# Optimization experiments

Hardware: AMD Instinct MI355X
Metric: run time of the kernel (lower is better)

Reference implementation:

```python
import jax, jax.numpy as jnp
import numpy as np

LN_EPS = 1e-5   # torch nn.LayerNorm default
OPM_EPS = 1e-3  # module eps


def _layer_norm(x, gamma, beta):
    mu = jnp.mean(x, axis=-1, keepdims=True)
    var = jnp.var(x, axis=-1, keepdims=True)
    return (x - mu) * jax.lax.rsqrt(var + LN_EPS) * gamma + beta


def setup_inputs() -> dict:
    key = jax.random.key(0)
    ks = jax.random.split(key, 4)
    S, N, c_m, c_h, c_z = 128, 384, 256, 32, 128
    return {
        "m": jax.random.normal(ks[0], (S, N, c_m), dtype=jnp.float32),
        "mask": jnp.ones((S, N), dtype=jnp.float32),
        "ln_gamma": jnp.ones((c_m,), dtype=jnp.float32),
        "ln_beta": jnp.zeros((c_m,), dtype=jnp.float32),
        "w1": jax.random.normal(ks[1], (c_m, c_h), dtype=jnp.float32) / np.sqrt(c_m),
        "b1": jnp.zeros((c_h,), dtype=jnp.float32),
        "w2": jax.random.normal(ks[2], (c_m, c_h), dtype=jnp.float32) / np.sqrt(c_m),
        "b2": jnp.zeros((c_h,), dtype=jnp.float32),
        "w_out": jax.random.normal(ks[3], (c_h * c_h, c_z), dtype=jnp.float32) / np.sqrt(c_h * c_h),
        "b_out": jnp.zeros((c_z,), dtype=jnp.float32),
    }


def reference(m, mask, ln_gamma, ln_beta, w1, b1, w2, b2, w_out, b_out):
    # m: [S, N, C_m], mask: [S, N]
    ln = _layer_norm(m, ln_gamma, ln_beta)                      # [S, N, C_m]
    a = (ln @ w1 + b1) * mask[..., None]                        # [S, N, C_h]
    b = (ln @ w2 + b2) * mask[..., None]                        # [S, N, C_h]
    a = jnp.swapaxes(a, -2, -3)                                 # [N, S, C_h]
    b = jnp.swapaxes(b, -2, -3)                                 # [N, S, C_h]
    norm = jnp.einsum('si,sj->ij', mask, mask)[..., None] + OPM_EPS  # [N, N, 1]
    outer = jnp.einsum('isc,jsd->ijcd', a, b)                   # [N, N, C_h, C_h]
    outer = outer.reshape(outer.shape[:-2] + (-1,))             # [N, N, C_h^2]
    out = outer @ w_out + b_out                                 # [N, N, C_z]
    return out / norm
```

## Files before the change

kernel.cpp:

```cpp
#include <hip/hip_runtime.h>
#include <hip/hip_bf16.h>

#define S_ 128
#define N_ 384
#define CM 256
#define CH 32
#define CZ 128

typedef __attribute__((ext_vector_type(8))) __bf16 bf16x8;
typedef __attribute__((ext_vector_type(4))) float f32x4;

union pack4 { __hip_bfloat16 h[4]; uint2 u; };

__global__ __launch_bounds__(384) void k_prep(const float* __restrict__ w1,
                                              const float* __restrict__ w2,
                                              const float* __restrict__ wout,
                                              const float* __restrict__ mask,
                                              __hip_bfloat16* __restrict__ wt12,
                                              __hip_bfloat16* __restrict__ woutT,
                                              float* __restrict__ RN)
{
    const int b = blockIdx.x, t = threadIdx.x;
    if (b < 64) {
        if (t < 256) {
            const float* w = (b < CH) ? w1 : w2;
            wt12[b * CM + t] = __float2bfloat16(w[(size_t)t * CH + (b & 31)]);
        }
    } else if (b < 192) {
        const int z = b - 64;
        for (int cd = t; cd < CH*CH; cd += 384)
            woutT[(size_t)z * (CH*CH) + cd] = __float2bfloat16(wout[(size_t)cd * CZ + z]);
    } else {
        const int i = b - 192, j = t;
        float acc = 0.f;
        #pragma unroll 8
        for (int s = 0; s < S_; ++s)
            acc += mask[s*N_ + i] * mask[s*N_ + j];
        RN[i*N_ + j] = 1.0f / (acc + 1e-3f);
    }
}

#define LNR 264
__global__ __launch_bounds__(256) void k_lnp(
    const float* __restrict__ m, const float* __restrict__ mask,
    const float* __restrict__ gamma, const float* __restrict__ beta,
    const float* __restrict__ b1, const float* __restrict__ b2,
    const __hip_bfloat16* __restrict__ wt12,
    __hip_bfloat16* __restrict__ At, __hip_bfloat16* __restrict__ Bt)
{
    __shared__ __hip_bfloat16 lnS[128 * LNR];
    __shared__ float msk[128];
    const int n0 = blockIdx.x * 16, s0 = blockIdx.y * 8;
    const int t = threadIdx.x, wave = t >> 6, lane = t & 63;
    const int l15 = lane & 15, quad = lane >> 4;

    if (t < 128) msk[t] = mask[(s0 + (t & 7))*N_ + n0 + (t >> 3)];

    float4 ga[4], be4[4];
    #pragma unroll
    for (int u = 0; u < 4; ++u) {
        ga[u]  = ((const float4*)gamma)[u*16 + l15];
        be4[u] = ((const float4*)beta )[u*16 + l15];
    }

    for (int it = 0; it < 8; ++it) {
        const int row = wave*32 + it*4 + quad;
        const int n = row >> 3, s = row & 7;
        const float4* src = (const float4*)(m + ((size_t)((s0+s)*N_ + n0 + n)) * CM);
        float4 x[4];
        #pragma unroll
        for (int u = 0; u < 4; ++u) x[u] = src[u*16 + l15];

        float sum = 0.f, ssq = 0.f;
        #pragma unroll
        for (int u = 0; u < 4; ++u) {
            sum += x[u].x + x[u].y + x[u].z + x[u].w;
            ssq += x[u].x*x[u].x + x[u].y*x[u].y + x[u].z*x[u].z + x[u].w*x[u].w;
        }
        #pragma unroll
        for (int off = 8; off >= 1; off >>= 1) {
            sum += __shfl_xor(sum, off, 64);
            ssq += __shfl_xor(ssq, off, 64);
        }
        const float mean = sum * (1.0f/CM);
        const float var  = ssq * (1.0f/CM) - mean*mean;
        const float rstd = rsqrtf(var + 1e-5f);

        #pragma unroll
        for (int u = 0; u < 4; ++u) {
            pack4 pk;
            pk.h[0] = __float2bfloat16((x[u].x - mean)*rstd*ga[u].x + be4[u].x);
            pk.h[1] = __float2bfloat16((x[u].y - mean)*rstd*ga[u].y + be4[u].y);
            pk.h[2] = __float2bfloat16((x[u].z - mean)*rstd*ga[u].z + be4[u].z);
            pk.h[3] = __float2bfloat16((x[u].w - mean)*rstd*ga[u].w + be4[u].w);
            *(uint2*)&lnS[row*LNR + (u*16 + l15)*4] = pk.u;
        }
    }
    __syncthreads();

    f32x4 acc[2][4];
    const f32x4 z4 = {0.f,0.f,0.f,0.f};
    #pragma unroll
    for (int mt = 0; mt < 2; ++mt)
        #pragma unroll
        for (int nt = 0; nt < 4; ++nt) acc[mt][nt] = z4;

    #pragma unroll
    for (int kk = 0; kk < 8; ++kk) {
        bf16x8 a0 = *(const bf16x8*)&lnS[(wave*32      + l15)*LNR + kk*32 + quad*8];
        bf16x8 a1 = *(const bf16x8*)&lnS[(wave*32 + 16 + l15)*LNR + kk*32 + quad*8];
        #pragma unroll
        for (int nt = 0; nt < 4; ++nt) {
            bf16x8 wv = *(const bf16x8*)&wt12[(size_t)(nt*16 + l15)*CM + kk*32 + quad*8];
            acc[0][nt] = __builtin_amdgcn_mfma_f32_16x16x32_bf16(a0, wv, acc[0][nt], 0,0,0);
            acc[1][nt] = __builtin_amdgcn_mfma_f32_16x16x32_bf16(a1, wv, acc[1][nt], 0,0,0);
        }
    }

    #pragma unroll
    for (int nt = 0; nt < 4; ++nt) {
        const int ncol = nt*16 + l15;
        const int sel = ncol >> 5, c = ncol & 31;
        const float bias = sel ? b2[c] : b1[c];
        __hip_bfloat16* dst = sel ? Bt : At;
        #pragma unroll
        for (int mt = 0; mt < 2; ++mt) {
            const int rowb = wave*32 + mt*16 + quad*4;
            const int n_loc = rowb >> 3, s_loc = rowb & 7;
            pack4 pk;
            #pragma unroll
            for (int r = 0; r < 4; ++r)
                pk.h[r] = __float2bfloat16((acc[mt][nt][r] + bias) * msk[rowb + r]);
            *(uint2*)&dst[((size_t)(n0 + n_loc)*CH + c)*S_ + s0 + s_loc] = pk.u;
        }
    }
}

#define OR 1160
__global__ __launch_bounds__(512) void k_opm(
    const __hip_bfloat16* __restrict__ At, const __hip_bfloat16* __restrict__ Bt,
    const float* __restrict__ RN, const __hip_bfloat16* __restrict__ woutT,
    const float* __restrict__ bout, float* __restrict__ out)
{
    __shared__ __hip_bfloat16 O[64 * OR];
    const int t = threadIdx.x;
    const int wave = t >> 6, lane = t & 63;
    const int l15 = lane & 15, quad = lane >> 4;
    const int i0 = blockIdx.x * 8, j0 = blockIdx.y * 8;
    const int mhalf = wave & 1, nquad = wave >> 1;

    f32x4 acc[4][8];
    const f32x4 z4 = {0.f,0.f,0.f,0.f};
    #pragma unroll
    for (int nt = 0; nt < 4; ++nt)
        #pragma unroll
        for (int mt = 0; mt < 8; ++mt) acc[nt][mt] = z4;

    const __hip_bfloat16* Ag[8];
    #pragma unroll
    for (int mt = 0; mt < 8; ++mt) {
        const int Mrow = mhalf*128 + mt*16 + l15;
        Ag[mt] = At + ((size_t)(i0 + (Mrow >> 5)) * CH + (Mrow & 31)) * S_ + quad*8;
    }
    const __hip_bfloat16* Bg[4];
    #pragma unroll
    for (int nt = 0; nt < 4; ++nt) {
        const int Ncol = nquad*64 + nt*16 + l15;
        Bg[nt] = Bt + ((size_t)(j0 + (Ncol >> 5)) * CH + (Ncol & 31)) * S_ + quad*8;
    }

    #pragma unroll
    for (int kk = 0; kk < 4; ++kk) {
        bf16x8 af[8], bfr[4];
        #pragma unroll
        for (int mt = 0; mt < 8; ++mt) af[mt] = *(const bf16x8*)(Ag[mt] + kk*32);
        #pragma unroll
        for (int nt = 0; nt < 4; ++nt) bfr[nt] = *(const bf16x8*)(Bg[nt] + kk*32);
        #pragma unroll
        for (int nt = 0; nt < 4; ++nt)
            #pragma unroll
            for (int mt = 0; mt < 8; ++mt)
                acc[nt][mt] = __builtin_amdgcn_mfma_f32_16x16x32_bf16(
                    bfr[nt], af[mt], acc[nt][mt], 0, 0, 0);
    }

    #pragma unroll
    for (int mt = 0; mt < 8; ++mt) {
        const int Mcol = mhalf*128 + mt*16 + l15;
        const int i_l = Mcol >> 5, c = Mcol & 31;
        #pragma unroll
        for (int nt = 0; nt < 4; ++nt) {
            const int Nrow = nquad*64 + nt*16 + quad*4;
            const int j_l = Nrow >> 5, d0 = Nrow & 31;
            const int p = i_l*8 + j_l;
            pack4 pk;
            #pragma unroll
            for (int r = 0; r < 4; ++r) pk.h[r] = __float2bfloat16(acc[nt][mt][r]);
            *(uint2*)&O[p*OR + c*36 + d0] = pk.u;
        }
    }
    __syncthreads();

    const int zb = wave * 16;
    f32x4 oacc[4];
    #pragma unroll
    for (int mt = 0; mt < 4; ++mt) oacc[mt] = z4;

    #pragma unroll
    for (int h = 0; h < 2; ++h) {
        bf16x8 wf[16];
        #pragma unroll
        for (int k2 = 0; k2 < 16; ++k2)
            wf[k2] = *(const bf16x8*)&woutT[(size_t)(zb + l15) * (CH*CH)
                                            + (h*16 + k2)*32 + quad*8];
        #pragma unroll
        for (int k2 = 0; k2 < 16; ++k2) {
            const int kk = h*16 + k2;
            #pragma unroll
            for (int mt = 0; mt < 4; ++mt) {
                bf16x8 a = *(const bf16x8*)&O[(mt*16 + l15)*OR + kk*36 + quad*8];
                oacc[mt] = __builtin_amdgcn_mfma_f32_16x16x32_bf16(
                    a, wf[k2], oacc[mt], 0, 0, 0);
            }
        }
    }

    const int zc = zb + l15;
    const float bz = bout[zc];
    #pragma unroll
    for (int mt = 0; mt < 4; ++mt) {
        #pragma unroll
        for (int r = 0; r < 4; ++r) {
            const int p = mt*16 + quad*4 + r;
            const int i = i0 + (p >> 3), j = j0 + (p & 7);
            const float rn = RN[i*N_ + j];
            out[((size_t)(i*N_ + j))*CZ + zc] = (oacc[mt][r] + bz) * rn;
        }
    }
}

extern "C" void kernel_launch(void* const* d_in, const int* in_sizes, int n_in,
                              void* d_out, int out_size, void* d_ws, size_t ws_size,
                              hipStream_t stream)
{
    const float* m    = (const float*)d_in[0];
    const float* mask = (const float*)d_in[1];
    const float* gam  = (const float*)d_in[2];
    const float* bet  = (const float*)d_in[3];
    const float* w1   = (const float*)d_in[4];
    const float* b1   = (const float*)d_in[5];
    const float* w2   = (const float*)d_in[6];
    const float* b2   = (const float*)d_in[7];
    const float* wout = (const float*)d_in[8];
    const float* bout = (const float*)d_in[9];
    float* out = (float*)d_out;

    __hip_bfloat16* At    = (__hip_bfloat16*)d_ws;
    __hip_bfloat16* Bt    = At + (size_t)N_ * CH * S_;
    __hip_bfloat16* woutT = Bt + (size_t)N_ * CH * S_;
    __hip_bfloat16* wt12  = woutT + (size_t)CZ * CH * CH;
    float*          RN    = (float*)(wt12 + (size_t)64 * CM);

    k_prep<<<576, 384, 0, stream>>>(w1, w2, wout, mask, wt12, woutT, RN);
    dim3 gl(24, 16);
    k_lnp<<<gl, 256, 0, stream>>>(m, mask, gam, bet, b1, b2, wt12, At, Bt);
    dim3 grid(N_ / 8, N_ / 8);
    k_opm<<<grid, 512, 0, stream>>>(At, Bt, RN, woutT, bout, out);
}
```

Before: 312.1 us.

## Split fused outer-product kernel into materialized outer tensor plus separate projection GEMM

```diff
diff --git a/kernel.cpp b/kernel.cpp
--- a/kernel.cpp
+++ b/kernel.cpp
@@ -136,6 +136,156 @@
     }
 }
 
+#define ONR 1160
+__global__ __launch_bounds__(256) void k_outer(
+    const __hip_bfloat16* __restrict__ At, const __hip_bfloat16* __restrict__ Bt,
+    __hip_bfloat16* __restrict__ Og, int i_base)
+{
+    __shared__ __hip_bfloat16 Ol[16 * ONR];
+    const int t = threadIdx.x;
+    const int wave = t >> 6, lane = t & 63;
+    const int l15 = lane & 15, quad = lane >> 4;
+    const int mhalf = wave & 1, nhalf = wave >> 1;
+    const int i0l = blockIdx.x * 4;
+    const int i0 = i_base + i0l;
+    const int j0 = blockIdx.y * 4;
+    const f32x4 z4 = {0.f,0.f,0.f,0.f};
+
+    f32x4 acc[4][4];
+    #pragma unroll
+    for (int nt = 0; nt < 4; ++nt)
+        #pragma unroll
+        for (int mt = 0; mt < 4; ++mt) acc[nt][mt] = z4;
+
+    const __hip_bfloat16* Ag[4];
+    #pragma unroll
+    for (int mt = 0; mt < 4; ++mt) {
+        const int Mrow = mhalf*64 + mt*16 + l15;
+        Ag[mt] = At + ((size_t)(i0 + (Mrow >> 5)) * CH + (Mrow & 31)) * S_ + quad*8;
+    }
+    const __hip_bfloat16* Bg[4];
+    #pragma unroll
+    for (int nt = 0; nt < 4; ++nt) {
+        const int Ncol = nhalf*64 + nt*16 + l15;
+        Bg[nt] = Bt + ((size_t)(j0 + (Ncol >> 5)) * CH + (Ncol & 31)) * S_ + quad*8;
+    }
+
+    #pragma unroll
+    for (int kk = 0; kk < 4; ++kk) {
+        bf16x8 af[4], bfr[4];
+        #pragma unroll
+        for (int mt = 0; mt < 4; ++mt) af[mt]  = *(const bf16x8*)(Ag[mt] + kk*32);
+        #pragma unroll
+        for (int nt = 0; nt < 4; ++nt) bfr[nt] = *(const bf16x8*)(Bg[nt] + kk*32);
+        #pragma unroll
+        for (int nt = 0; nt < 4; ++nt)
+            #pragma unroll
+            for (int mt = 0; mt < 4; ++mt)
+                acc[nt][mt] = __builtin_amdgcn_mfma_f32_16x16x32_bf16(
+                    bfr[nt], af[mt], acc[nt][mt], 0, 0, 0);
+    }
+
+    #pragma unroll
+    for (int mt = 0; mt < 4; ++mt) {
+        const int Mcol = mhalf*64 + mt*16 + l15;
+        const int i_l = Mcol >> 5, c = Mcol & 31;
+        #pragma unroll
+        for (int nt = 0; nt < 4; ++nt) {
+            const int Nrow = nhalf*64 + nt*16 + quad*4;
+            const int j_l = Nrow >> 5, d0 = Nrow & 31;
+            const int p = i_l*4 + j_l;
+            pack4 pk;
+            #pragma unroll
+            for (int r = 0; r < 4; ++r) pk.h[r] = __float2bfloat16(acc[nt][mt][r]);
+            *(uint2*)&Ol[p*ONR + c*36 + d0] = pk.u;
+        }
+    }
+    __syncthreads();
+
+    #pragma unroll
+    for (int ps = 0; ps < 8; ++ps) {
+        const int g  = ps*2048 + t*8;
+        const int p  = g >> 10, cd = g & 1023;
+        const int c  = cd >> 5, d = cd & 31;
+        const int pi = p >> 2,  pj = p & 3;
+        uint2 a0 = *(const uint2*)&Ol[p*ONR + c*36 + d];
+        uint2 a1 = *(const uint2*)&Ol[p*ONR + c*36 + d + 4];
+        uint4 v; v.x = a0.x; v.y = a0.y; v.z = a1.x; v.w = a1.y;
+        *(uint4*)&Og[((size_t)(i0l + pi)*N_ + (j0 + pj))*1024 + cd] = v;
+    }
+}
+
+__global__ __launch_bounds__(256) void k_wo(
+    const __hip_bfloat16* __restrict__ Og, const __hip_bfloat16* __restrict__ woutT,
+    const float* __restrict__ RN, const float* __restrict__ bout,
+    float* __restrict__ out, int p_base)
+{
+    __shared__ __hip_bfloat16 As[128 * 132];
+    const int t = threadIdx.x;
+    const int wave = t >> 6, lane = t & 63;
+    const int l15 = lane & 15, quad = lane >> 4;
+    const int p0 = blockIdx.x * 128;
+    const f32x4 z4 = {0.f,0.f,0.f,0.f};
+
+    f32x4 acc[2][8];
+    #pragma unroll
+    for (int mt = 0; mt < 2; ++mt)
+        #pragma unroll
+        for (int nt = 0; nt < 8; ++nt) acc[mt][nt] = z4;
+
+    for (int kc = 0; kc < 8; ++kc) {
+        uint4 ld[8];
+        #pragma unroll
+        for (int ps = 0; ps < 8; ++ps) {
+            const int idx = ps*256 + t;
+            const int r = idx >> 4, colb = (idx & 15)*8;
+            ld[ps] = *(const uint4*)&Og[((size_t)(p0 + r))*1024 + kc*128 + colb];
+        }
+        __syncthreads();
+        #pragma unroll
+        for (int ps = 0; ps < 8; ++ps) {
+            const int idx = ps*256 + t;
+            const int r = idx >> 4, colb = (idx & 15)*8;
+            *(uint4*)&As[r*132 + colb] = ld[ps];
+        }
+        __syncthreads();
+
+        #pragma unroll
+        for (int kk = 0; kk < 4; ++kk) {
+            bf16x8 a[2];
+            #pragma unroll
+            for (int mt = 0; mt < 2; ++mt)
+                a[mt] = *(const bf16x8*)&As[(wave*32 + mt*16 + l15)*132 + kk*32 + quad*8];
+            bf16x8 wf[8];
+            #pragma unroll
+            for (int nt = 0; nt < 8; ++nt)
+                wf[nt] = *(const bf16x8*)&woutT[(size_t)(nt*16 + l15)*(CH*CH)
+                                                + kc*128 + kk*32 + quad*8];
+            #pragma unroll
+            for (int mt = 0; mt < 2; ++mt)
+                #pragma unroll
+                for (int nt = 0; nt < 8; ++nt)
+                    acc[mt][nt] = __builtin_amdgcn_mfma_f32_16x16x32_bf16(
+                        a[mt], wf[nt], acc[mt][nt], 0, 0, 0);
+        }
+    }
+
+    #pragma unroll
+    for (int nt = 0; nt < 8; ++nt) {
+        const int z = nt*16 + l15;
+        const float bz = bout[z];
+        #pragma unroll
+        for (int mt = 0; mt < 2; ++mt) {
+            #pragma unroll
+            for (int r = 0; r < 4; ++r) {
+                const int p_loc = p0 + wave*32 + mt*16 + quad*4 + r;
+                const int pg = p_base + p_loc;
+                out[(size_t)pg*CZ + z] = (acc[mt][nt][r] + bz) * RN[pg];
+            }
+        }
+    }
+}
+
 #define OR 1160
 __global__ __launch_bounds__(512) void k_opm(
     const __hip_bfloat16* __restrict__ At, const __hip_bfloat16* __restrict__ Bt,
@@ -260,10 +410,30 @@
     __hip_bfloat16* woutT = Bt + (size_t)N_ * CH * S_;
     __hip_bfloat16* wt12  = woutT + (size_t)CZ * CH * CH;
     float*          RN    = (float*)(wt12 + (size_t)64 * CM);
+    const size_t base = (size_t)N_*CH*S_*2*2 + (size_t)CZ*CH*CH*2
+                      + (size_t)64*CM*2 + (size_t)N_*N_*4;
 
     k_prep<<<576, 384, 0, stream>>>(w1, w2, wout, mask, wt12, woutT, RN);
     dim3 gl(24, 16);
     k_lnp<<<gl, 256, 0, stream>>>(m, mask, gam, bet, b1, b2, wt12, At, Bt);
-    dim3 grid(N_ / 8, N_ / 8);
-    k_opm<<<grid, 512, 0, stream>>>(At, Bt, RN, woutT, bout, out);
-}
+
+    int CI = 0;
+    const int cands[3] = {384, 192, 96};
+    for (int c = 0; c < 3; ++c) {
+        const size_t need = base + (size_t)cands[c] * N_ * 1024 * 2;
+        if (need <= ws_size) { CI = cands[c]; break; }
+    }
+
+    if (CI) {
+        __hip_bfloat16* Og = (__hip_bfloat16*)((char*)d_ws + base);
+        const int nch = N_ / CI;
+        for (int c = 0; c < nch; ++c) {
+            dim3 go(CI/4, 96);
+            k_outer<<<go, 256, 0, stream>>>(At, Bt, Og, c*CI);
+            k_wo<<<CI*3, 256, 0, stream>>>(Og, woutT, RN, bout, out, c*CI*N_);
+        }
+    } else {
+        dim3 grid(N_ / 8, N_ / 8);
+        k_opm<<<grid, 512, 0, stream>>>(At, Bt, RN, woutT, bout, out);
+    }
+}
```

Result: slower. 568.4 us (+82.1%).
